# Performance work log

Hardware: AMD Instinct MI355X
Metric: run time of the kernel (lower is better)

The kernel has to match this reference:

```python
import jax, jax.numpy as jnp
import numpy as np

N = 50000
E = 400000
IN = 128
OUT = 128
HID = 32
HEADS = 8
NEG_SLOPE = 0.2

_DIMS_IN = [IN, HID * HEADS, HID * HEADS, HID * HEADS]
_HEADS = [HEADS, HEADS, HEADS, 1]
_CH = [HID, HID, HID, OUT]


def setup_inputs() -> dict:
    key = jax.random.key(0)
    ks = list(jax.random.split(key, 32))
    kit = iter(ks)

    def p(shape, s=0.05):
        return (jax.random.normal(next(kit), shape, dtype=jnp.float32) * s)

    inp = {}
    inp["x"] = jax.random.normal(next(kit), (N, IN), dtype=jnp.float32)
    inp["edge_index"] = jax.random.randint(next(kit), (2, E), 0, N, dtype=jnp.int32)
    for i in range(4):
        hc = _HEADS[i] * _CH[i]
        inp[f"Wl{i}"] = p((hc, _DIMS_IN[i]))
        inp[f"bl{i}"] = p((hc,))
        inp[f"Wr{i}"] = p((hc, _DIMS_IN[i]))
        inp[f"br{i}"] = p((hc,))
        inp[f"att{i}"] = p((_HEADS[i], _CH[i]))
        inp[f"b{i}"] = p((hc,))
    return inp


def _gatv2_conv(x, src, dst, Wl, bl, Wr, br, att, bias, concat):
    # PyG GATv2Conv (share_weights=False, add_self_loops handled by caller).
    n = x.shape[0]
    H, C = att.shape
    xl = (x @ Wl.T + bl).reshape(n, H, C)  # source-side transform
    xr = (x @ Wr.T + br).reshape(n, H, C)  # dest-side transform
    e = jax.nn.leaky_relu(xl[src] + xr[dst], NEG_SLOPE)  # [E, H, C]
    logits = jnp.einsum('ehc,hc->eh', e, att)            # [E, H]
    # per-destination softmax (numerically stable via segment max)
    m = jax.ops.segment_max(logits, dst, num_segments=n)
    p = jnp.exp(logits - m[dst])
    denom = jax.ops.segment_sum(p, dst, num_segments=n)
    alpha = p / denom[dst]                                # [E, H]
    out = jax.ops.segment_sum(alpha[:, :, None] * xl[src], dst, num_segments=n)  # [N, H, C]
    out = out.reshape(n, H * C) if concat else out.mean(axis=1)
    return out + bias


def reference(x, edge_index, Wl0, bl0, Wr0, br0, att0, b0,
              Wl1, bl1, Wr1, br1, att1, b1,
              Wl2, bl2, Wr2, br2, att2, b2,
              Wl3, bl3, Wr3, br3, att3, b3):
    loop = jnp.arange(N, dtype=edge_index.dtype)  # default add_self_loops=True
    src = jnp.concatenate([edge_index[0], loop])
    dst = jnp.concatenate([edge_index[1], loop])
    layers = [
        (Wl0, bl0, Wr0, br0, att0, b0, True),
        (Wl1, bl1, Wr1, br1, att1, b1, True),
        (Wl2, bl2, Wr2, br2, att2, b2, True),
        (Wl3, bl3, Wr3, br3, att3, b3, False),
    ]
    h = x
    for params in layers[:-1]:
        res = h
        h = _gatv2_conv(h, src, dst, *params)
        h = jax.nn.elu(h)  # dropout is identity in eval mode
        if res.shape == h.shape:
            h = h + res
    return _gatv2_conv(h, src, dst, *layers[-1])
```

## Files before the change

### kernel.cpp

```cpp
#include <hip/hip_runtime.h>
#include <hip/hip_bf16.h>

constexpr int NN = 50000;
constexpr int NE = 400000;
constexpr int NE2 = NE + NN;
constexpr float NEG_SLOPE = 0.2f;
constexpr float LOG2E = 1.44269504f;

typedef __attribute__((ext_vector_type(8))) __bf16 bf16x8;
typedef __attribute__((ext_vector_type(4))) float f32x4;
typedef __attribute__((ext_vector_type(2))) float f32x2;

__device__ inline float bf2f(unsigned short u) { return __uint_as_float(((unsigned)u) << 16); }
__device__ inline unsigned short f2bf(float f) {
    unsigned x = __float_as_uint(f);
    return (unsigned short)((x + 0x7fffu + ((x >> 16) & 1u)) >> 16);
}
__device__ inline float bflo(unsigned u) { return __uint_as_float(u << 16); }
__device__ inline float bfhi(unsigned u) { return __uint_as_float(u & 0xffff0000u); }

__device__ inline void gload16(const unsigned short* g, unsigned short* l) {
    __builtin_amdgcn_global_load_lds(
        (const __attribute__((address_space(1))) unsigned int*)(g),
        (__attribute__((address_space(3))) unsigned int*)(l), 16, 0, 0);
}

__global__ void count_deg(const int* __restrict__ ei, int* __restrict__ deg) {
    int e = blockIdx.x * blockDim.x + threadIdx.x;
    if (e >= NE2) return;
    int dst = (e < NE) ? ei[NE + e] : (e - NE);
    atomicAdd(&deg[dst], 1);
}

__global__ __launch_bounds__(1024) void scan_deg(const int* __restrict__ deg,
                                                 int* __restrict__ row_ptr,
                                                 int* __restrict__ cursor) {
    constexpr int CH = (NN + 1023) / 1024;
    __shared__ int wsum[16];
    const int t = threadIdx.x, lane = t & 63, w = t >> 6;
    const int base = t * CH;
    int v[CH];
    int s = 0;
    #pragma unroll
    for (int i = 0; i < CH; ++i) {
        int idx = base + i;
        int dv = (idx < NN) ? deg[idx] : 0;
        v[i] = s;
        s += dv;
    }
    int x = s;
    #pragma unroll
    for (int off = 1; off < 64; off <<= 1) {
        int y = __shfl_up(x, off);
        if (lane >= off) x += y;
    }
    if (lane == 63) wsum[w] = x;
    __syncthreads();
    if (w == 0 && lane < 16) {
        int ss = wsum[lane];
        #pragma unroll
        for (int off = 1; off < 16; off <<= 1) {
            int y = __shfl_up(ss, off);
            if (lane >= off) ss += y;
        }
        wsum[lane] = ss;
    }
    __syncthreads();
    const int excl = ((w == 0) ? 0 : wsum[w - 1]) + (x - s);
    #pragma unroll
    for (int i = 0; i < CH; ++i) {
        int idx = base + i;
        if (idx < NN) { int e = excl + v[i]; row_ptr[idx] = e; cursor[idx] = e; }
    }
    if (t == 0) row_ptr[NN] = wsum[15];
}

__global__ void scatter_edges(const int* __restrict__ ei, int* __restrict__ cursor,
                              int* __restrict__ csr_src) {
    int e = blockIdx.x * blockDim.x + threadIdx.x;
    if (e >= NE2) return;
    int src, dst;
    if (e < NE) { src = ei[e]; dst = ei[NE + e]; }
    else        { src = dst = e - NE; }
    int pos = atomicAdd(&cursor[dst], 1);
    csr_src[pos] = src;
}

__global__ void f32_to_bf16(const float* __restrict__ in, unsigned short* __restrict__ out, int n4) {
    int i = blockIdx.x * blockDim.x + threadIdx.x;
    if (i >= n4) return;
    float4 v = *(const float4*)(in + 4 * (size_t)i);
    ushort4 o;
    o.x = f2bf(v.x); o.y = f2bf(v.y); o.z = f2bf(v.z); o.w = f2bf(v.w);
    *(ushort4*)(out + 4 * (size_t)i) = o;
}

__global__ void conv_weights(const float* __restrict__ w0l, const float* __restrict__ w0r,
                             const float* __restrict__ w1l, const float* __restrict__ w1r,
                             const float* __restrict__ w2l, const float* __restrict__ w2r,
                             const float* __restrict__ w3l, const float* __restrict__ w3r,
                             unsigned short* __restrict__ out) {
    int i = blockIdx.x * blockDim.x + threadIdx.x;
    const float* src; int base;
    if      (i < 8192)  { src = w0l; base = 0; }
    else if (i < 16384) { src = w0r; base = 8192; }
    else if (i < 32768) { src = w1l; base = 16384; }
    else if (i < 49152) { src = w1r; base = 32768; }
    else if (i < 65536) { src = w2l; base = 49152; }
    else if (i < 81920) { src = w2r; base = 65536; }
    else if (i < 90112) { src = w3l; base = 81920; }
    else                { src = w3r; base = 90112; }
    float4 v = ((const float4*)src)[i - base];
    ushort4 o;
    o.x = f2bf(v.x); o.y = f2bf(v.y); o.z = f2bf(v.z); o.w = f2bf(v.w);
    ((ushort4*)out)[i] = o;
}

#define GBM 128
#define GBN 128
#define GBK 64

__global__ __launch_bounds__(256) void gemm_fused(const unsigned short* __restrict__ A,
                                                  const unsigned short* __restrict__ Wc,
                                                  const float* __restrict__ bl,
                                                  const float* __restrict__ br,
                                                  unsigned short* __restrict__ outl,
                                                  unsigned short* __restrict__ outr,
                                                  int M, int Nhalf, int K, int lognx) {
    __shared__ __align__(16) unsigned short Alds[2][GBM * GBK];
    __shared__ __align__(16) unsigned short Wlds[2][GBN * GBK];
    const int nwg = gridDim.x;
    const int q = nwg >> 3, r8 = nwg & 7;
    const int xcd = blockIdx.x & 7, off = blockIdx.x >> 3;
    const int wg = (xcd < r8 ? xcd * (q + 1) : r8 * (q + 1) + (xcd - r8) * q) + off;
    const int nx = 1 << lognx;
    const int bm = (wg >> lognx) * GBM, bn = (wg & (nx - 1)) * GBN;

    const int tid = threadIdx.x;
    const int lane = tid & 63, wave = tid >> 6;
    const int wr = wave >> 1, wc = wave & 1;
    const int lrow = lane & 15, kgrp = lane >> 4;

    f32x4 acc[4][4] = {};

    auto stage = [&](int cur, int k0) {
        #pragma unroll
        for (int i = 0; i < 4; ++i) {
            int p = i * 256 + tid;
            int r = p >> 3, ck = p & 7;
            int sck = ck ^ (r & 7);
            int ga = bm + r; ga = (ga < M) ? ga : (M - 1);
            gload16(A + (size_t)ga * K + k0 + sck * 8,
                    &Alds[cur][(unsigned)(i * 256 + wave * 64) * 8]);
            gload16(Wc + (size_t)(bn + r) * K + k0 + sck * 8,
                    &Wlds[cur][(unsigned)(i * 256 + wave * 64) * 8]);
        }
    };

    const int nt = K >> 6;
    stage(0, 0);
    __syncthreads();
    int cur = 0;
    for (int t = 0; t < nt; ++t) {
        if (t + 1 < nt) stage(cur ^ 1, (t + 1) * GBK);
        const unsigned short* Ab = Alds[cur];
        const unsigned short* Wb = Wlds[cur];
        #pragma unroll
        for (int kk = 0; kk < GBK; kk += 32) {
            bf16x8 av[4], bv[4];
            #pragma unroll
            for (int i = 0; i < 4; ++i) {
                int ar = wr * 64 + i * 16 + lrow;
                int ch = ((kk >> 3) + kgrp) ^ (ar & 7);
                av[i] = *(const bf16x8*)(&Ab[ar * GBK + ch * 8]);
            }
            #pragma unroll
            for (int j = 0; j < 4; ++j) {
                int brw = wc * 64 + j * 16 + lrow;
                int ch = ((kk >> 3) + kgrp) ^ (brw & 7);
                bv[j] = *(const bf16x8*)(&Wb[brw * GBK + ch * 8]);
            }
            #pragma unroll
            for (int i = 0; i < 4; ++i)
                #pragma unroll
                for (int j = 0; j < 4; ++j)
                    acc[i][j] = __builtin_amdgcn_mfma_f32_16x16x32_bf16(bv[j], av[i], acc[i][j], 0, 0, 0);
        }
        __syncthreads();
        cur ^= 1;
    }

    const int half = (bn >= Nhalf) ? 1 : 0;
    unsigned short* outp = half ? outr : outl;
    const float* bp = half ? br : bl;
    const int cb = bn - half * Nhalf + wc * 64;
    #pragma unroll
    for (int i = 0; i < 4; ++i) {
        int row = bm + wr * 64 + i * 16 + lrow;
        if (row < M) {
            #pragma unroll
            for (int j = 0; j < 4; ++j) {
                int col = cb + j * 16 + kgrp * 4;
                float4 bb = *(const float4*)(bp + col);
                ushort4 o;
                o.x = f2bf(acc[i][j][0] + bb.x);
                o.y = f2bf(acc[i][j][1] + bb.y);
                o.z = f2bf(acc[i][j][2] + bb.z);
                o.w = f2bf(acc[i][j][3] + bb.w);
                *(ushort4*)(outp + (size_t)row * Nhalf + col) = o;
            }
        }
    }
}

template <int HC, int C, bool DO_ELU, bool DO_RES, bool OUT_F32>
__global__ __launch_bounds__(128) void gat_edge8(
        const unsigned short* __restrict__ xl,
        const unsigned short* __restrict__ xr,
        const float* __restrict__ att, const float* __restrict__ bias,
        const unsigned short* __restrict__ res, void* __restrict__ outp,
        const int* __restrict__ row_ptr, const int* __restrict__ csr_src) {
    constexpr int T = HC / 8;
    constexpr int NSL = 64 / T;
    constexpr int RW = C / 8;
    constexpr float THR = 11.54f;

    const int lane = threadIdx.x & 63;
    const int n = __builtin_amdgcn_readfirstlane((blockIdx.x << 1) | (threadIdx.x >> 6));
    const int w = lane / T;
    const int t = lane % T;
    const int ch = t * 8;
    const size_t base_r = (size_t)n * HC + ch;

    f32x2 xr2[4], av2[4], acc2[4];
    {
        uint4 u = *(const uint4*)(xr + base_r);
        xr2[0] = f32x2{bflo(u.x), bfhi(u.x)};
        xr2[1] = f32x2{bflo(u.y), bfhi(u.y)};
        xr2[2] = f32x2{bflo(u.z), bfhi(u.z)};
        xr2[3] = f32x2{bflo(u.w), bfhi(u.w)};
        float4 a0 = *(const float4*)(att + ch);
        float4 a1 = *(const float4*)(att + ch + 4);
        av2[0] = f32x2{a0.x, a0.y} * LOG2E;
        av2[1] = f32x2{a0.z, a0.w} * LOG2E;
        av2[2] = f32x2{a1.x, a1.y} * LOG2E;
        av2[3] = f32x2{a1.z, a1.w} * LOG2E;
        #pragma unroll
        for (int qi = 0; qi < 4; ++qi) acc2[qi] = f32x2{0.f, 0.f};
    }

    float m = -1e30f, d = 0.f;
    const int beg = row_ptr[n], end = row_ptr[n + 1];
    int e = beg + w;
    for (; e + NSL < end; e += 2 * NSL) {
        int s0 = csr_src[e], s1 = csr_src[e + NSL];
        uint4 g0 = *(const uint4*)(xl + (size_t)s0 * HC + ch);
        uint4 g1 = *(const uint4*)(xl + (size_t)s1 * HC + ch);
        f32x2 x0[4], x1[4];
        x0[0] = f32x2{bflo(g0.x), bfhi(g0.x)}; x0[1] = f32x2{bflo(g0.y), bfhi(g0.y)};
        x0[2] = f32x2{bflo(g0.z), bfhi(g0.z)}; x0[3] = f32x2{bflo(g0.w), bfhi(g0.w)};
        x1[0] = f32x2{bflo(g1.x), bfhi(g1.x)}; x1[1] = f32x2{bflo(g1.y), bfhi(g1.y)};
        x1[2] = f32x2{bflo(g1.z), bfhi(g1.z)}; x1[3] = f32x2{bflo(g1.w), bfhi(g1.w)};
        f32x2 p02 = {0.f, 0.f}, p12 = {0.f, 0.f};
        #pragma unroll
        for (int qi = 0; qi < 4; ++qi) {
            f32x2 u0 = x0[qi] + xr2[qi];
            f32x2 t0 = u0 * NEG_SLOPE;
            u0.x = fmaxf(u0.x, t0.x); u0.y = fmaxf(u0.y, t0.y);
            p02 = u0 * av2[qi] + p02;
            f32x2 u1 = x1[qi] + xr2[qi];
            f32x2 t1 = u1 * NEG_SLOPE;
            u1.x = fmaxf(u1.x, t1.x); u1.y = fmaxf(u1.y, t1.y);
            p12 = u1 * av2[qi] + p12;
        }
        float p0 = p02.x + p02.y, p1 = p12.x + p12.y;
        #pragma unroll
        for (int mm = RW / 2; mm >= 1; mm >>= 1) {
            p0 += __shfl_xor(p0, mm);
            p1 += __shfl_xor(p1, mm);
        }
        float pmax = fmaxf(p0, p1);
        if (__any(pmax > m + THR)) {
            float mn = fmaxf(m, pmax);
            float sc = exp2f(m - mn);
            float e0 = exp2f(p0 - mn), e1 = exp2f(p1 - mn);
            d = d * sc + e0 + e1;
            f32x2 sc2 = {sc, sc}, e02 = {e0, e0}, e12 = {e1, e1};
            #pragma unroll
            for (int qi = 0; qi < 4; ++qi)
                acc2[qi] = acc2[qi] * sc2 + (x0[qi] * e02 + x1[qi] * e12);
            m = mn;
        } else {
            float e0 = exp2f(p0 - m), e1 = exp2f(p1 - m);
            d += e0 + e1;
            f32x2 e02 = {e0, e0}, e12 = {e1, e1};
            #pragma unroll
            for (int qi = 0; qi < 4; ++qi)
                acc2[qi] = acc2[qi] + (x0[qi] * e02 + x1[qi] * e12);
        }
    }
    if (e < end) {
        int s0 = csr_src[e];
        uint4 g0 = *(const uint4*)(xl + (size_t)s0 * HC + ch);
        f32x2 x0[4];
        x0[0] = f32x2{bflo(g0.x), bfhi(g0.x)}; x0[1] = f32x2{bflo(g0.y), bfhi(g0.y)};
        x0[2] = f32x2{bflo(g0.z), bfhi(g0.z)}; x0[3] = f32x2{bflo(g0.w), bfhi(g0.w)};
        f32x2 p02 = {0.f, 0.f};
        #pragma unroll
        for (int qi = 0; qi < 4; ++qi) {
            f32x2 u0 = x0[qi] + xr2[qi];
            f32x2 t0 = u0 * NEG_SLOPE;
            u0.x = fmaxf(u0.x, t0.x); u0.y = fmaxf(u0.y, t0.y);
            p02 = u0 * av2[qi] + p02;
        }
        float p0 = p02.x + p02.y;
        #pragma unroll
        for (int mm = RW / 2; mm >= 1; mm >>= 1) p0 += __shfl_xor(p0, mm);
        if (__any(p0 > m + THR)) {
            float mn = fmaxf(m, p0);
            float sc = exp2f(m - mn);
            float e0 = exp2f(p0 - mn);
            d = d * sc + e0;
            f32x2 sc2 = {sc, sc}, e02 = {e0, e0};
            #pragma unroll
            for (int qi = 0; qi < 4; ++qi) acc2[qi] = acc2[qi] * sc2 + x0[qi] * e02;
            m = mn;
        } else {
            float e0 = exp2f(p0 - m);
            d += e0;
            f32x2 e02 = {e0, e0};
            #pragma unroll
            for (int qi = 0; qi < 4; ++qi) acc2[qi] = acc2[qi] + x0[qi] * e02;
        }
    }

    #pragma unroll
    for (int st = T; st < 64; st <<= 1) {
        float mo = __shfl_xor(m, st);
        float do_ = __shfl_xor(d, st);
        float ao[8];
        #pragma unroll
        for (int qi = 0; qi < 4; ++qi) {
            ao[2 * qi]     = __shfl_xor(acc2[qi].x, st);
            ao[2 * qi + 1] = __shfl_xor(acc2[qi].y, st);
        }
        float mn = fmaxf(m, mo);
        float s0 = exp2f(m - mn), s1 = exp2f(mo - mn);
        d = d * s0 + do_ * s1;
        #pragma unroll
        for (int qi = 0; qi < 4; ++qi) {
            acc2[qi].x = acc2[qi].x * s0 + ao[2 * qi] * s1;
            acc2[qi].y = acc2[qi].y * s0 + ao[2 * qi + 1] * s1;
        }
        m = mn;
    }

    if (lane < T) {
        float inv = 1.f / d;
        float o[8];
        float4 b0 = *(const float4*)(bias + ch);
        float4 b1 = *(const float4*)(bias + ch + 4);
        o[0] = acc2[0].x * inv + b0.x; o[1] = acc2[0].y * inv + b0.y;
        o[2] = acc2[1].x * inv + b0.z; o[3] = acc2[1].y * inv + b0.w;
        o[4] = acc2[2].x * inv + b1.x; o[5] = acc2[2].y * inv + b1.y;
        o[6] = acc2[3].x * inv + b1.z; o[7] = acc2[3].y * inv + b1.w;
        if constexpr (DO_ELU) {
            #pragma unroll
            for (int v = 0; v < 8; ++v)
                o[v] = o[v] > 0.f ? o[v] : exp2f(o[v] * LOG2E) - 1.f;
        }
        if constexpr (DO_RES) {
            uint4 ru = *(const uint4*)(res + base_r);
            o[0] += bflo(ru.x); o[1] += bfhi(ru.x);
            o[2] += bflo(ru.y); o[3] += bfhi(ru.y);
            o[4] += bflo(ru.z); o[5] += bfhi(ru.z);
            o[6] += bflo(ru.w); o[7] += bfhi(ru.w);
        }
        if constexpr (OUT_F32) {
            float* op = (float*)outp + base_r;
            *(float4*)(op)     = make_float4(o[0], o[1], o[2], o[3]);
            *(float4*)(op + 4) = make_float4(o[4], o[5], o[6], o[7]);
        } else {
            uint4 u;
            u.x = (unsigned)f2bf(o[0]) | ((unsigned)f2bf(o[1]) << 16);
            u.y = (unsigned)f2bf(o[2]) | ((unsigned)f2bf(o[3]) << 16);
            u.z = (unsigned)f2bf(o[4]) | ((unsigned)f2bf(o[5]) << 16);
            u.w = (unsigned)f2bf(o[6]) | ((unsigned)f2bf(o[7]) << 16);
            *(uint4*)((unsigned short*)outp + base_r) = u;
        }
    }
}

extern "C" void kernel_launch(void* const* d_in, const int* in_sizes, int n_in,
                              void* d_out, int out_size, void* d_ws, size_t ws_size,
                              hipStream_t stream) {
    const float* x  = (const float*)d_in[0];
    const int*   ei = (const int*)d_in[1];
    auto P = [&](int layer, int j) { return (const float*)d_in[2 + 6 * layer + j]; };

    unsigned short* x_bf = (unsigned short*)d_ws;
    unsigned short* h0 = x_bf + (size_t)NN * 128;
    unsigned short* h1 = h0 + (size_t)NN * 256;
    unsigned short* xl = h1 + (size_t)NN * 256;
    unsigned short* xr = xl + (size_t)NN * 256;
    unsigned short* Wb = xr + (size_t)NN * 256;
    int* csr_src = (int*)(Wb + 393216);
    int* row_ptr = csr_src + NE2;
    int* cursor  = row_ptr + (NN + 1);
    int* deg     = cursor + NN;

    hipMemsetAsync(deg, 0, NN * sizeof(int), stream);
    int eb = (NE2 + 255) / 256;
    count_deg<<<eb, 256, 0, stream>>>(ei, deg);
    scan_deg<<<1, 1024, 0, stream>>>(deg, row_ptr, cursor);
    scatter_edges<<<eb, 256, 0, stream>>>(ei, cursor, csr_src);

    conv_weights<<<384, 256, 0, stream>>>(P(0, 0), P(0, 2), P(1, 0), P(1, 2),
                                          P(2, 0), P(2, 2), P(3, 0), P(3, 2), Wb);
    int n4 = NN * 128 / 4;
    f32_to_bf16<<<(n4 + 255) / 256, 256, 0, stream>>>(x, x_bf, n4);

    const int mb = (NN + GBM - 1) / GBM;
    const int nwgL = 4 * mb, nwgLast = 2 * mb;
    const int gat_g = NN / 2;

    gemm_fused<<<nwgL, 256, 0, stream>>>(x_bf, Wb + 0,      P(0, 1), P(0, 3), xl, xr, NN, 256, 128, 2);
    gat_edge8<256, 32, true, false, false><<<gat_g, 128, 0, stream>>>(xl, xr, P(0, 4), P(0, 5),
                                                                      nullptr, h0, row_ptr, csr_src);
    gemm_fused<<<nwgL, 256, 0, stream>>>(h0,   Wb + 65536,  P(1, 1), P(1, 3), xl, xr, NN, 256, 256, 2);
    gat_edge8<256, 32, true, true, false><<<gat_g, 128, 0, stream>>>(xl, xr, P(1, 4), P(1, 5),
                                                                     h0, h1, row_ptr, csr_src);
    gemm_fused<<<nwgL, 256, 0, stream>>>(h1,   Wb + 196608, P(2, 1), P(2, 3), xl, xr, NN, 256, 256, 2);
    gat_edge8<256, 32, true, true, false><<<gat_g, 128, 0, stream>>>(xl, xr, P(2, 4), P(2, 5),
                                                                     h1, h0, row_ptr, csr_src);
    gemm_fused<<<nwgLast, 256, 0, stream>>>(h0, Wb + 327680, P(3, 1), P(3, 3), xl, xr, NN, 128, 256, 1);
    gat_edge8<128, 128, false, false, true><<<gat_g, 128, 0, stream>>>(xl, xr, P(3, 4), P(3, 5),
                                                                       nullptr, d_out, row_ptr, csr_src);
}
```

Baseline: 468.4 us.

## Split degree scan into multi-block passes and single-buffer GEMM LDS staging

Replaces the single-workgroup degree prefix scan with a three-kernel scan: per-block local scans, a scan of the block sums, and an add-back pass. This spreads the scan across many CUs instead of serialising it on one. Separately, the GEMM drops LDS double buffering and loads each K tile synchronously before computing on it. That halves LDS use, which may raise occupancy, but it gives up the overlap of global loads with MFMA work.

```diff
diff --git a/kernel.cpp b/kernel.cpp
--- a/kernel.cpp
+++ b/kernel.cpp
@@ -32,23 +32,16 @@
     atomicAdd(&deg[dst], 1);
 }
 
-__global__ __launch_bounds__(1024) void scan_deg(const int* __restrict__ deg,
-                                                 int* __restrict__ row_ptr,
-                                                 int* __restrict__ cursor) {
-    constexpr int CH = (NN + 1023) / 1024;
+constexpr int SCAN_NB = (NN + 1023) / 1024;
+
+__global__ __launch_bounds__(1024) void scan_local(const int* __restrict__ deg,
+                                                   int* __restrict__ row_ptr,
+                                                   int* __restrict__ bsum) {
     __shared__ int wsum[16];
     const int t = threadIdx.x, lane = t & 63, w = t >> 6;
-    const int base = t * CH;
-    int v[CH];
-    int s = 0;
-    #pragma unroll
-    for (int i = 0; i < CH; ++i) {
-        int idx = base + i;
-        int dv = (idx < NN) ? deg[idx] : 0;
-        v[i] = s;
-        s += dv;
-    }
-    int x = s;
+    const int i = blockIdx.x * 1024 + t;
+    int v = (i < NN) ? deg[i] : 0;
+    int x = v;
     #pragma unroll
     for (int off = 1; off < 64; off <<= 1) {
         int y = __shfl_up(x, off);
@@ -57,22 +50,42 @@
     if (lane == 63) wsum[w] = x;
     __syncthreads();
     if (w == 0 && lane < 16) {
-        int ss = wsum[lane];
+        int s = wsum[lane];
         #pragma unroll
         for (int off = 1; off < 16; off <<= 1) {
-            int y = __shfl_up(ss, off);
-            if (lane >= off) ss += y;
-        }
-        wsum[lane] = ss;
+            int y = __shfl_up(s, off);
+            if (lane >= off) s += y;
+        }
+        wsum[lane] = s;
     }
     __syncthreads();
-    const int excl = ((w == 0) ? 0 : wsum[w - 1]) + (x - s);
+    int excl = ((w == 0) ? 0 : wsum[w - 1]) + x - v;
+    if (i < NN) row_ptr[i] = excl;
+    if (t == 1023) bsum[blockIdx.x] = wsum[15];
+}
+
+__global__ void scan_bsums(int* __restrict__ bsum, int* __restrict__ row_ptr) {
+    int lane = threadIdx.x;
+    int v = (lane < SCAN_NB) ? bsum[lane] : 0;
+    int x = v;
     #pragma unroll
-    for (int i = 0; i < CH; ++i) {
-        int idx = base + i;
-        if (idx < NN) { int e = excl + v[i]; row_ptr[idx] = e; cursor[idx] = e; }
-    }
-    if (t == 0) row_ptr[NN] = wsum[15];
+    for (int off = 1; off < 64; off <<= 1) {
+        int y = __shfl_up(x, off);
+        if (lane >= off) x += y;
+    }
+    if (lane < SCAN_NB) bsum[lane] = x - v;
+    if (lane == 63) row_ptr[NN] = x;
+}
+
+__global__ __launch_bounds__(1024) void scan_add(int* __restrict__ row_ptr,
+                                                 int* __restrict__ cursor,
+                                                 const int* __restrict__ bsum) {
+    const int i = blockIdx.x * 1024 + threadIdx.x;
+    if (i < NN) {
+        int e = row_ptr[i] + bsum[blockIdx.x];
+        row_ptr[i] = e;
+        cursor[i] = e;
+    }
 }
 
 __global__ void scatter_edges(const int* __restrict__ ei, int* __restrict__ cursor,
@@ -127,8 +140,8 @@
                                                   unsigned short* __restrict__ outl,
                                                   unsigned short* __restrict__ outr,
                                                   int M, int Nhalf, int K, int lognx) {
-    __shared__ __align__(16) unsigned short Alds[2][GBM * GBK];
-    __shared__ __align__(16) unsigned short Wlds[2][GBN * GBK];
+    __shared__ __align__(16) unsigned short Alds[GBM * GBK];
+    __shared__ __align__(16) unsigned short Wlds[GBN * GBK];
     const int nwg = gridDim.x;
     const int q = nwg >> 3, r8 = nwg & 7;
     const int xcd = blockIdx.x & 7, off = blockIdx.x >> 3;
@@ -143,28 +156,19 @@
 
     f32x4 acc[4][4] = {};
 
-    auto stage = [&](int cur, int k0) {
+    for (int k0 = 0; k0 < K; k0 += GBK) {
         #pragma unroll
         for (int i = 0; i < 4; ++i) {
             int p = i * 256 + tid;
             int r = p >> 3, ck = p & 7;
             int sck = ck ^ (r & 7);
             int ga = bm + r; ga = (ga < M) ? ga : (M - 1);
-            gload16(A + (size_t)ga * K + k0 + sck * 8,
-                    &Alds[cur][(unsigned)(i * 256 + wave * 64) * 8]);
-            gload16(Wc + (size_t)(bn + r) * K + k0 + sck * 8,
-                    &Wlds[cur][(unsigned)(i * 256 + wave * 64) * 8]);
-        }
-    };
-
-    const int nt = K >> 6;
-    stage(0, 0);
-    __syncthreads();
-    int cur = 0;
-    for (int t = 0; t < nt; ++t) {
-        if (t + 1 < nt) stage(cur ^ 1, (t + 1) * GBK);
-        const unsigned short* Ab = Alds[cur];
-        const unsigned short* Wb = Wlds[cur];
+            unsigned short* la = &Alds[(unsigned)(i * 256 + wave * 64) * 8];
+            gload16(A + (size_t)ga * K + k0 + sck * 8, la);
+            unsigned short* lw = &Wlds[(unsigned)(i * 256 + wave * 64) * 8];
+            gload16(Wc + (size_t)(bn + r) * K + k0 + sck * 8, lw);
+        }
+        __syncthreads();
         #pragma unroll
         for (int kk = 0; kk < GBK; kk += 32) {
             bf16x8 av[4], bv[4];
@@ -172,13 +176,13 @@
             for (int i = 0; i < 4; ++i) {
                 int ar = wr * 64 + i * 16 + lrow;
                 int ch = ((kk >> 3) + kgrp) ^ (ar & 7);
-                av[i] = *(const bf16x8*)(&Ab[ar * GBK + ch * 8]);
+                av[i] = *(const bf16x8*)(&Alds[ar * GBK + ch * 8]);
             }
             #pragma unroll
             for (int j = 0; j < 4; ++j) {
                 int brw = wc * 64 + j * 16 + lrow;
                 int ch = ((kk >> 3) + kgrp) ^ (brw & 7);
-                bv[j] = *(const bf16x8*)(&Wb[brw * GBK + ch * 8]);
+                bv[j] = *(const bf16x8*)(&Wlds[brw * GBK + ch * 8]);
             }
             #pragma unroll
             for (int i = 0; i < 4; ++i)
@@ -187,7 +191,6 @@
                     acc[i][j] = __builtin_amdgcn_mfma_f32_16x16x32_bf16(bv[j], av[i], acc[i][j], 0, 0, 0);
         }
         __syncthreads();
-        cur ^= 1;
     }
 
     const int half = (bn >= Nhalf) ? 1 : 0;
@@ -408,11 +411,14 @@
     int* row_ptr = csr_src + NE2;
     int* cursor  = row_ptr + (NN + 1);
     int* deg     = cursor + NN;
+    int* bsum    = deg + NN;
 
     hipMemsetAsync(deg, 0, NN * sizeof(int), stream);
     int eb = (NE2 + 255) / 256;
     count_deg<<<eb, 256, 0, stream>>>(ei, deg);
-    scan_deg<<<1, 1024, 0, stream>>>(deg, row_ptr, cursor);
+    scan_local<<<SCAN_NB, 1024, 0, stream>>>(deg, row_ptr, bsum);
+    scan_bsums<<<1, 64, 0, stream>>>(bsum, row_ptr);
+    scan_add<<<SCAN_NB, 1024, 0, stream>>>(row_ptr, cursor, bsum);
     scatter_edges<<<eb, 256, 0, stream>>>(ei, cursor, csr_src);
 
     conv_weights<<<384, 256, 0, stream>>>(P(0, 0), P(0, 2), P(1, 0), P(1, 2),
```

Result: faster. 395.4 us (-15.6%).
